# Kernel optimization log

Measured on AMD Instinct MI355X. Metric: run time of the kernel, lower is better.

The kernel has to match this reference:

```python
import jax, jax.numpy as jnp
import numpy as np

SEQ_LEN = 2048
BATCH = 32
HIDDEN = 1
MLP_HID = 256
OUT_DIM = 1


def setup_inputs() -> dict:
    key = jax.random.key(0)
    ks = jax.random.split(key, 12)
    d = {
        "src": jax.random.normal(ks[0], (SEQ_LEN, BATCH), dtype=jnp.float32),
        "Wq": jax.random.normal(ks[1], (HIDDEN, HIDDEN), dtype=jnp.float32),
        "bq": jax.random.normal(ks[2], (HIDDEN,), dtype=jnp.float32) * 0.1,
        "Wk": jax.random.normal(ks[3], (HIDDEN, HIDDEN), dtype=jnp.float32),
        "bk": jax.random.normal(ks[4], (HIDDEN,), dtype=jnp.float32) * 0.1,
        "Wv": jax.random.normal(ks[5], (HIDDEN, HIDDEN), dtype=jnp.float32),
        "bv": jax.random.normal(ks[6], (HIDDEN,), dtype=jnp.float32) * 0.1,
        "bias": jax.random.normal(ks[7], (1, SEQ_LEN, SEQ_LEN), dtype=jnp.float32),
        "W1": jax.random.normal(ks[8], (MLP_HID, HIDDEN), dtype=jnp.float32) * (1.0 / np.sqrt(HIDDEN)),
        "b1": jax.random.normal(ks[9], (MLP_HID,), dtype=jnp.float32) * 0.1,
        "W2": jax.random.normal(ks[10], (OUT_DIM, MLP_HID), dtype=jnp.float32) * (1.0 / np.sqrt(MLP_HID)),
        "b2": jax.random.normal(ks[11], (OUT_DIM,), dtype=jnp.float32) * 0.1,
    }
    return d


def reference(src, Wq, bq, Wk, bk, Wv, bv, bias, W1, b1, W2, b2):
    # src: [S, B] -> x: [S, B, H] with H == 1 (forced by unsqueeze(2) + Linear)
    x = src[..., None]
    # Linear projections, then transpose(0,1) -> [B, S, H]
    q = jnp.swapaxes(jnp.einsum('sbh,oh->sbo', x, Wq) + bq, 0, 1)
    k = jnp.swapaxes(jnp.einsum('sbh,oh->sbo', x, Wk) + bk, 0, 1)
    v = jnp.swapaxes(jnp.einsum('sbh,oh->sbo', x, Wv) + bv, 0, 1)
    # QK^T / sqrt(H) + learned additive bias: [B, S, S]
    scores = jnp.einsum('bsh,bth->bst', q, k) / jnp.sqrt(jnp.float32(HIDDEN)) + bias
    attn = jax.nn.softmax(scores, axis=-1)  # has_softmax=True
    # attn @ V -> [B, S, H], transpose back -> [S, B, H]
    ctx = jnp.swapaxes(jnp.einsum('bst,bth->bsh', attn, v), 0, 1)
    # 2-layer ReLU MLP on last dim
    h = jax.nn.relu(jnp.einsum('sbh,mh->sbm', ctx, W1) + b1)
    y = jnp.einsum('sbm,om->sbo', h, W2) + b2  # [S, B, OUT_DIM]
    return y[0, :, 0]  # [B]
```

## Files before the change

kernel.cpp:

```cpp
#include <hip/hip_runtime.h>
#include <math.h>


constexpr int S   = 2048;
constexpr int B   = 32;
constexpr int TPB = 256;
constexpr int TPT = S / TPB;

__global__ __launch_bounds__(TPB) void fused_transformer_row0(
    const float* __restrict__ src,
    const float* __restrict__ Wq, const float* __restrict__ bq,
    const float* __restrict__ Wk, const float* __restrict__ bk,
    const float* __restrict__ Wv, const float* __restrict__ bv,
    const float* __restrict__ bias,
    const float* __restrict__ W1,
    const float* __restrict__ b1,
    const float* __restrict__ W2,
    const float* __restrict__ b2,
    float* __restrict__ out)
{
    const int b    = blockIdx.x;
    const int tid  = threadIdx.x;
    const int lane = tid & 63;
    const int wave = tid >> 6;

    __shared__ float red_m[4];
    __shared__ float red_l[4];
    __shared__ float red_c[4];
    __shared__ float red_y[4];

    const float wq  = Wq[0], wk = Wk[0], wv = Wv[0];
    const float bk0 = bk[0], bv0 = bv[0];
    const float qb = src[0 * B + b] * wq + bq[0];

    float sc[TPT], vv[TPT];
    float mloc = -INFINITY;
#pragma unroll
    for (int i = 0; i < TPT; ++i) {
        const int t = tid + i * TPB;
        const float x = src[t * B + b];
        sc[i] = qb * (x * wk + bk0) + bias[t];
        vv[i] = x * wv + bv0;
        mloc  = fmaxf(mloc, sc[i]);
    }

#pragma unroll
    for (int off = 32; off > 0; off >>= 1)
        mloc = fmaxf(mloc, __shfl_down(mloc, off, 64));
    if (lane == 0) red_m[wave] = mloc;
    __syncthreads();
    const float gmax = fmaxf(fmaxf(red_m[0], red_m[1]), fmaxf(red_m[2], red_m[3]));

    float lsum = 0.f, csum = 0.f;
#pragma unroll
    for (int i = 0; i < TPT; ++i) {
        const float e = __expf(sc[i] - gmax);
        lsum += e;
        csum += e * vv[i];
    }
#pragma unroll
    for (int off = 32; off > 0; off >>= 1) {
        lsum += __shfl_down(lsum, off, 64);
        csum += __shfl_down(csum, off, 64);
    }
    if (lane == 0) { red_l[wave] = lsum; red_c[wave] = csum; }
    __syncthreads();
    const float L = red_l[0] + red_l[1] + red_l[2] + red_l[3];
    const float C = red_c[0] + red_c[1] + red_c[2] + red_c[3];
    const float ctx = C / L;

    float h = fmaxf(ctx * W1[tid] + b1[tid], 0.f);
    float term = h * W2[tid];
#pragma unroll
    for (int off = 32; off > 0; off >>= 1)
        term += __shfl_down(term, off, 64);
    __syncthreads();
    if (lane == 0) red_y[wave] = term;
    __syncthreads();
    if (tid == 0)
        out[b] = red_y[0] + red_y[1] + red_y[2] + red_y[3] + b2[0];
}

extern "C" void kernel_launch(void* const* d_in, const int* in_sizes, int n_in,
                              void* d_out, int out_size, void* d_ws, size_t ws_size,
                              hipStream_t stream) {
    const float* src  = (const float*)d_in[0];
    const float* Wq   = (const float*)d_in[1];
    const float* bq   = (const float*)d_in[2];
    const float* Wk   = (const float*)d_in[3];
    const float* bk   = (const float*)d_in[4];
    const float* Wv   = (const float*)d_in[5];
    const float* bv   = (const float*)d_in[6];
    const float* bias = (const float*)d_in[7];
    const float* W1   = (const float*)d_in[8];
    const float* b1   = (const float*)d_in[9];
    const float* W2   = (const float*)d_in[10];
    const float* b2   = (const float*)d_in[11];
    float* out = (float*)d_out;

    fused_transformer_row0<<<B, TPB, 0, stream>>>(
        src, Wq, bq, Wk, bk, Wv, bv, bias, W1, b1, W2, b2, out);
}
```

Before: 86.63 us.

## Collapse to a single 1024-thread block with coalesced src reads across batch

Replaces the per-batch grid of 32 blocks with one 1024-thread block where lanes map to batch index, so src loads become coalesced rows and bias is read once instead of 32 times. The softmax is recomputed in two passes over src/bias instead of holding scores in registers. This cuts uncoalesced strided global loads and redundant bias traffic but runs on a single CU, giving up parallelism across the device.

```diff
diff --git a/kernel.cpp b/kernel.cpp
--- a/kernel.cpp
+++ b/kernel.cpp
@@ -4,8 +4,9 @@
 
 constexpr int S   = 2048;
 constexpr int B   = 32;
-constexpr int TPB = 256;
-constexpr int TPT = S / TPB;
+constexpr int TPB = 1024;
+constexpr int NW  = TPB / 64;
+constexpr int ITER = S / (TPB / B);
 
 __global__ __launch_bounds__(TPB) void fused_transformer_row0(
     const float* __restrict__ src,
@@ -19,66 +20,81 @@
     const float* __restrict__ b2,
     float* __restrict__ out)
 {
-    const int b    = blockIdx.x;
     const int tid  = threadIdx.x;
+    const int b    = tid & 31;
+    const int g    = tid >> 5;
     const int lane = tid & 63;
     const int wave = tid >> 6;
 
-    __shared__ float red_m[4];
-    __shared__ float red_l[4];
-    __shared__ float red_c[4];
-    __shared__ float red_y[4];
+    __shared__ float redA[NW * 32];
+    __shared__ float redB[NW * 32];
+    __shared__ float finM[32];
+    __shared__ float finCtx[32];
 
     const float wq  = Wq[0], wk = Wk[0], wv = Wv[0];
-    const float bk0 = bk[0], bv0 = bv[0];
-    const float qb = src[0 * B + b] * wq + bq[0];
+    const float bq0 = bq[0], bk0 = bk[0], bv0 = bv[0];
+    const float qb  = src[b] * wq + bq0;
 
-    float sc[TPT], vv[TPT];
     float mloc = -INFINITY;
-#pragma unroll
-    for (int i = 0; i < TPT; ++i) {
-        const int t = tid + i * TPB;
-        const float x = src[t * B + b];
-        sc[i] = qb * (x * wk + bk0) + bias[t];
-        vv[i] = x * wv + bv0;
-        mloc  = fmaxf(mloc, sc[i]);
+#pragma unroll 8
+    for (int i = 0; i < ITER; ++i) {
+        const int idx = tid + TPB * i;
+        const int t   = g + 32 * i;
+        const float x = src[idx];
+        const float s = qb * (x * wk + bk0) + bias[t];
+        mloc = fmaxf(mloc, s);
     }
-
-#pragma unroll
-    for (int off = 32; off > 0; off >>= 1)
-        mloc = fmaxf(mloc, __shfl_down(mloc, off, 64));
-    if (lane == 0) red_m[wave] = mloc;
+    mloc = fmaxf(mloc, __shfl_down(mloc, 32, 64));
+    if (lane < 32) redA[wave * 32 + b] = mloc;
     __syncthreads();
-    const float gmax = fmaxf(fmaxf(red_m[0], red_m[1]), fmaxf(red_m[2], red_m[3]));
+    if (tid < 32) {
+        float m = redA[tid];
+        for (int w = 1; w < NW; ++w) m = fmaxf(m, redA[w * 32 + tid]);
+        finM[tid] = m;
+    }
+    __syncthreads();
+    const float gmax = finM[b];
 
     float lsum = 0.f, csum = 0.f;
+#pragma unroll 8
+    for (int i = 0; i < ITER; ++i) {
+        const int idx = tid + TPB * i;
+        const int t   = g + 32 * i;
+        const float x = src[idx];
+        const float s = qb * (x * wk + bk0) + bias[t];
+        const float e = __expf(s - gmax);
+        lsum += e;
+        csum += e * (x * wv + bv0);
+    }
+    lsum += __shfl_down(lsum, 32, 64);
+    csum += __shfl_down(csum, 32, 64);
+    __syncthreads();
+    if (lane < 32) { redA[wave * 32 + b] = lsum; redB[wave * 32 + b] = csum; }
+    __syncthreads();
+    if (tid < 32) {
+        float L = 0.f, C = 0.f;
+        for (int w = 0; w < NW; ++w) { L += redA[w * 32 + tid]; C += redB[w * 32 + tid]; }
+        finCtx[tid] = C / L;
+    }
+    __syncthreads();
+    const float ctx = finCtx[b];
+
+    float term = 0.f;
 #pragma unroll
-    for (int i = 0; i < TPT; ++i) {
-        const float e = __expf(sc[i] - gmax);
-        lsum += e;
-        csum += e * vv[i];
+    for (int j = 0; j < 8; ++j) {
+        const int m   = g + 32 * j;
+        const float h = fmaxf(ctx * W1[m] + b1[m], 0.f);
+        term += h * W2[m];
     }
-#pragma unroll
-    for (int off = 32; off > 0; off >>= 1) {
-        lsum += __shfl_down(lsum, off, 64);
-        csum += __shfl_down(csum, off, 64);
+    term += __shfl_down(term, 32, 64);
+    __syncthreads();
+    if (lane < 32) redA[wave * 32 + b] = term;
+    __syncthreads();
+    if (tid < 32) {
+        float s = 0.f;
+        for (int w = 0; w < NW; ++w) s += redA[w * 32 + tid];
+        out[tid] = s + b2[0];
     }
-    if (lane == 0) { red_l[wave] = lsum; red_c[wave] = csum; }
-    __syncthreads();
-    const float L = red_l[0] + red_l[1] + red_l[2] + red_l[3];
-    const float C = red_c[0] + red_c[1] + red_c[2] + red_c[3];
-    const float ctx = C / L;
-
-    float h = fmaxf(ctx * W1[tid] + b1[tid], 0.f);
-    float term = h * W2[tid];
-#pragma unroll
-    for (int off = 32; off > 0; off >>= 1)
-        term += __shfl_down(term, off, 64);
-    __syncthreads();
-    if (lane == 0) red_y[wave] = term;
-    __syncthreads();
-    if (tid == 0)
-        out[b] = red_y[0] + red_y[1] + red_y[2] + red_y[3] + b2[0];
 }
 
 extern "C" void kernel_launch(void* const* d_in, const int* in_sizes, int n_in,
@@ -98,6 +114,6 @@
     const float* b2   = (const float*)d_in[11];
     float* out = (float*)d_out;
 
-    fused_transformer_row0<<<B, TPB, 0, stream>>>(
+    fused_transformer_row0<<<1, TPB, 0, stream>>>(
         src, Wq, bq, Wk, bk, Wv, bv, bias, W1, b1, W2, b2, out);
 }
```

New measurement: 99.10 us. 14.4% more time.
